# Performance work log

Hardware: AMD Instinct MI355X
Metric: run time of the kernel (lower is better)

## Reference

```python
import jax, jax.numpy as jnp
import numpy as np

N_NODES = 50000
N_EDGES = 100000
NUM_GRAPHS = 1024
EMB = 600
NUM_ATOMIC = 119      # Num_atomic_number
NUM_HYB = 8           # HybridizationType values
NUM_AROM = 2
NUM_CHIR = 4          # ChiralType values
NUM_CHARGE = 9
NUM_BOND_TYPE = 22    # BondType values


def setup_inputs() -> dict:
    key = jax.random.key(0)
    ks = jax.random.split(key, 20)
    # integer graph data
    atom = jnp.stack([
        jax.random.randint(ks[0], (N_NODES,), 0, NUM_ATOMIC),
        jax.random.randint(ks[1], (N_NODES,), 0, NUM_HYB),
        jax.random.randint(ks[2], (N_NODES,), 0, NUM_AROM),
        jax.random.randint(ks[3], (N_NODES,), 0, NUM_CHIR),
        jax.random.randint(ks[4], (N_NODES,), 0, NUM_CHARGE),
    ], axis=1)
    bond_index = jax.random.randint(ks[5], (2, N_EDGES), 0, N_NODES)
    bond_attr = jnp.stack([
        jax.random.randint(ks[6], (N_EDGES,), 0, NUM_BOND_TYPE),
        jax.random.randint(ks[7], (N_EDGES,), 0, NUM_ATOMIC),
    ], axis=1)
    batch = jnp.sort(jax.random.randint(ks[8], (N_NODES,), 0, NUM_GRAPHS))
    # parameters (kaiming-uniform-ish scale)
    def emb(k, n, d):
        bound = float(np.sqrt(6.0 / d))
        return jax.random.uniform(k, (n, d), minval=-bound, maxval=bound, dtype=jnp.float32)
    def lin(k, out_d, in_d):
        bound = float(np.sqrt(6.0 / in_d))
        return jax.random.uniform(k, (out_d, in_d), minval=-bound, maxval=bound, dtype=jnp.float32)
    return {
        "atom": atom, "bond_index": bond_index, "bond_attr": bond_attr, "batch": batch,
        "W_atom_num": emb(ks[9], NUM_ATOMIC, EMB),
        "W_hyb": emb(ks[10], NUM_HYB, EMB),
        "W_arom": emb(ks[11], NUM_AROM, EMB),
        "W_chir": emb(ks[12], NUM_CHIR, EMB),
        "W_charge": emb(ks[13], NUM_CHARGE, EMB),
        "W_bond_type": emb(ks[14], NUM_BOND_TYPE, EMB),
        "W_bond_atom_i": emb(ks[15], NUM_ATOMIC, EMB),
        "W_sl_atom": emb(ks[16], NUM_ATOMIC, EMB),
        "W_sl": emb(ks[17], 1, EMB),
        "W1": lin(ks[18], EMB, EMB), "b1": jnp.zeros((EMB,), jnp.float32),
        "W2": lin(ks[19], EMB // 2, EMB), "b2": jnp.zeros((EMB // 2,), jnp.float32),
        "W3": lin(jax.random.fold_in(key, 99), 1, EMB // 2),
    }


def reference(atom, bond_index, bond_attr, batch,
              W_atom_num, W_hyb, W_arom, W_chir, W_charge,
              W_bond_type, W_bond_atom_i, W_sl_atom, W_sl,
              W1, b1, W2, b2, W3):
    N = atom.shape[0]
    # Step 1: node embedding = sum of 5 lookups  [N, EMB]
    node = (W_atom_num[atom[:, 0]] + W_hyb[atom[:, 1]] + W_arom[atom[:, 2]]
            + W_chir[atom[:, 3]] + W_charge[atom[:, 4]])
    # Step 2: edge embeddings; self-loops appended after real bonds
    bond_emb = W_bond_type[bond_attr[:, 0]] + W_bond_atom_i[bond_attr[:, 1]]  # [E, EMB]
    sl_emb = W_sl_atom[atom[:, 0]] + W_sl[0]                                  # [N, EMB]
    edge_emb = jnp.concatenate([bond_emb, sl_emb], axis=0)                    # [E+N, EMB]
    loop = jnp.arange(N, dtype=bond_index.dtype)
    src = jnp.concatenate([bond_index[0], loop])
    dst = jnp.concatenate([bond_index[1], loop])
    # Step 3: 2 message-passing layers: gather src, multiply edge_emb, scatter-add to dst
    for _ in range(2):
        node = jax.ops.segment_sum(node[src] * edge_emb, dst, num_segments=N)
    # Step 4: energy MLP  ReLU -> Linear(d,d) -> ReLU -> Linear(d,d/2) -> ReLU -> Linear(d/2,1)
    h = jax.nn.relu(node)
    h = jax.nn.relu(h @ W1.T + b1)
    h = jax.nn.relu(h @ W2.T + b2)
    node_energy = h @ W3.T  # [N, 1]
    # Step 5: global add pool per graph
    dg = jax.ops.segment_sum(node_energy, batch, num_segments=NUM_GRAPHS)  # [NUM_GRAPHS, 1]
    return dg
```

## Files before the change

### kernel.cpp

```cpp
#include <hip/hip_runtime.h>

#define EMB 600
#define Q4  150
#define KP  608

typedef unsigned short ushortT;
typedef __attribute__((ext_vector_type(8))) short short8;
typedef __attribute__((ext_vector_type(4))) short short4v;
typedef __attribute__((ext_vector_type(4))) float f32x4;

__device__ __forceinline__ float4 f4add(float4 a, float4 b) {
    return make_float4(a.x + b.x, a.y + b.y, a.z + b.z, a.w + b.w);
}
__device__ __forceinline__ float4 f4fma(float4 acc, float4 v, float4 e) {
    return make_float4(fmaf(v.x, e.x, acc.x), fmaf(v.y, e.y, acc.y),
                       fmaf(v.z, e.z, acc.z), fmaf(v.w, e.w, acc.w));
}
__device__ __forceinline__ ushortT bf16_rne(float x) {
    unsigned u = __float_as_uint(x);
    return (ushortT)((u + 0x7fffu + ((u >> 16) & 1u)) >> 16);
}
__device__ __forceinline__ float bf16_to_f(ushortT h) {
    return __uint_as_float(((unsigned)h) << 16);
}
__device__ __forceinline__ short4v f4_to_bf4(float4 v) {
    short4v r;
    r[0] = (short)bf16_rne(v.x);
    r[1] = (short)bf16_rne(v.y);
    r[2] = (short)bf16_rne(v.z);
    r[3] = (short)bf16_rne(v.w);
    return r;
}
__device__ __forceinline__ float4 bf4_to_f4(short4v h) {
    return make_float4(bf16_to_f((ushortT)h[0]), bf16_to_f((ushortT)h[1]),
                       bf16_to_f((ushortT)h[2]), bf16_to_f((ushortT)h[3]));
}

__device__ __forceinline__ size_t frag_off(int row, int col) {
    return ((size_t)((row >> 4) * 19 + (col >> 5)) * 64
            + (row & 15) + 16 * ((col >> 3) & 3)) * 8 + (col & 7);
}

__global__ void k_node_embed_b(const int* __restrict__ atom,
                               const float4* __restrict__ Wa,
                               const float4* __restrict__ Wh,
                               const float4* __restrict__ War,
                               const float4* __restrict__ Wc,
                               const float4* __restrict__ Wch,
                               ushortT* __restrict__ out, int N) {
    int idx = blockIdx.x * blockDim.x + threadIdx.x;
    int total = N * Q4;
    if (idx >= total) return;
    int n = idx / Q4;
    int q = idx - n * Q4;
    const int* a = atom + n * 5;
    float4 r = Wa[a[0] * Q4 + q];
    r = f4add(r, Wh [a[1] * Q4 + q]);
    r = f4add(r, War[a[2] * Q4 + q]);
    r = f4add(r, Wc [a[3] * Q4 + q]);
    r = f4add(r, Wch[a[4] * Q4 + q]);
    *(short4v*)(out + (size_t)n * EMB + q * 4) = f4_to_bf4(r);
}

__global__ void k_hist(const int* __restrict__ bdst, int* __restrict__ counts, int E) {
    int i = blockIdx.x * blockDim.x + threadIdx.x;
    if (i < E) atomicAdd(&counts[bdst[i]], 1);
}

__global__ __launch_bounds__(256) void k_scan_l1(const int* __restrict__ counts,
                                                 int* __restrict__ offsets,
                                                 int* __restrict__ blocksums, int N) {
    __shared__ int s[256];
    int t = threadIdx.x;
    int i = blockIdx.x * 256 + t;
    int v = (i < N) ? counts[i] : 0;
    s[t] = v;
    __syncthreads();
#pragma unroll
    for (int off = 1; off < 256; off <<= 1) {
        int x = (t >= off) ? s[t - off] : 0;
        __syncthreads();
        s[t] += x;
        __syncthreads();
    }
    if (i < N) offsets[i] = s[t] - v;
    if (t == 255) blocksums[blockIdx.x] = s[255];
}

__global__ __launch_bounds__(256) void k_scan_l2(int* __restrict__ blocksums,
                                                 int* __restrict__ blockpref, int nb) {
    __shared__ int s[256];
    int t = threadIdx.x;
    int v = (t < nb) ? blocksums[t] : 0;
    s[t] = v;
    __syncthreads();
#pragma unroll
    for (int off = 1; off < 256; off <<= 1) {
        int x = (t >= off) ? s[t - off] : 0;
        __syncthreads();
        s[t] += x;
        __syncthreads();
    }
    if (t < nb) blockpref[t] = s[t] - v;
}

__global__ __launch_bounds__(256) void k_scan_l3(int* __restrict__ offsets,
                                                 int* __restrict__ cursor,
                                                 const int* __restrict__ blockpref, int N) {
    int i = blockIdx.x * 256 + threadIdx.x;
    if (i < N) {
        int o = offsets[i] + blockpref[blockIdx.x];
        offsets[i] = o;
        cursor[i]  = o;
    }
}

__global__ void k_scatter(const int* __restrict__ bdst, int* __restrict__ cursor,
                          int* __restrict__ edge_list, int E) {
    int i = blockIdx.x * blockDim.x + threadIdx.x;
    if (i < E) {
        int pos = atomicAdd(&cursor[bdst[i]], 1);
        edge_list[pos] = i;
    }
}

#define MP_BODY                                                                \
    int start = offsets[d], cnt = counts[d];                                   \
    int s0 = 0, t00 = 0, t01 = 0, s1 = 0, t10 = 0, t11 = 0;                    \
    if (cnt > 0) {                                                             \
        int e = edge_list[start];                                              \
        s0 = bsrc[e]; t00 = battr[2 * e]; t01 = battr[2 * e + 1];              \
    }                                                                          \
    if (cnt > 1) {                                                             \
        int e = edge_list[start + 1];                                          \
        s1 = bsrc[e]; t10 = battr[2 * e]; t11 = battr[2 * e + 1];              \
    }                                                                          \
    short4v cs1 = {0, 0, 0, 0}, cs2 = {0, 0, 0, 0};                            \
    if (cnt > 0) {                                                             \
        const ushortT* sr = in + (size_t)s0 * EMB;                             \
        cs1 = *(const short4v*)(sr + q1 * 4);                                  \
        if (has2) cs2 = *(const short4v*)(sr + q2 * 4);                        \
    }                                                                          \
    const float4* slA = Wsla + atom[d * 5] * Q4;                               \
    const ushortT* inr = in + (size_t)d * EMB;                                 \
    float4 acc1 = make_float4(0, 0, 0, 0), acc2 = acc1;                        \
    acc1 = f4fma(acc1, bf4_to_f4(*(const short4v*)(inr + q1 * 4)),             \
                 f4add(slA[q1], Wsl[q1]));                                     \
    if (has2) acc2 = f4fma(acc2, bf4_to_f4(*(const short4v*)(inr + q2 * 4)),   \
                           f4add(slA[q2], Wsl[q2]));                           \
    for (int k = 0; k < cnt; k++) {                                            \
        short4v xs1 = cs1, xs2 = cs2;                                          \
        int ct0 = t00, ct1 = t01;                                              \
        s0 = s1; t00 = t10; t01 = t11;                                         \
        if (k + 2 < cnt) {                                                     \
            int e = edge_list[start + k + 2];                                  \
            s1 = bsrc[e]; t10 = battr[2 * e]; t11 = battr[2 * e + 1];          \
        }                                                                      \
        if (k + 1 < cnt) {                                                     \
            const ushortT* sr = in + (size_t)s0 * EMB;                         \
            cs1 = *(const short4v*)(sr + q1 * 4);                              \
            if (has2) cs2 = *(const short4v*)(sr + q2 * 4);                    \
        }                                                                      \
        const float4* e0 = Wbt  + ct0 * Q4;                                    \
        const float4* e1 = Wbai + ct1 * Q4;                                    \
        acc1 = f4fma(acc1, bf4_to_f4(xs1), f4add(e0[q1], e1[q1]));             \
        if (has2) acc2 = f4fma(acc2, bf4_to_f4(xs2), f4add(e0[q2], e1[q2]));   \
    }

__global__ __launch_bounds__(256) void k_mp_gather_b(
        const int* __restrict__ bsrc, const int* __restrict__ battr,
        const int* __restrict__ atom,
        const int* __restrict__ offsets, const int* __restrict__ counts,
        const int* __restrict__ edge_list,
        const float4* __restrict__ Wbt, const float4* __restrict__ Wbai,
        const float4* __restrict__ Wsla, const float4* __restrict__ Wsl,
        const ushortT* __restrict__ in, ushortT* __restrict__ out, int N) {
    int wid  = (int)((blockIdx.x * blockDim.x + threadIdx.x) >> 6);
    int lane = threadIdx.x & 63;
    int d    = wid >> 1;
    int half = wid & 1;
    if (d >= N) return;
    int q1 = 75 * half + lane;
    int q2 = q1 + 64;
    bool has2 = lane < 11;

    MP_BODY

    ushortT* orow = out + (size_t)d * EMB;
    *(short4v*)(orow + q1 * 4) = f4_to_bf4(acc1);
    if (has2) *(short4v*)(orow + q2 * 4) = f4_to_bf4(acc2);
}

__device__ __forceinline__ void frag_store4h(ushortT* __restrict__ hi,
                                             int d, int q, float4 v) {
    int kc = q >> 3, ks = (q >> 1) & 3, halfw = q & 1;
    size_t off = ((size_t)((d >> 4) * 19 + kc) * 64 + (d & 15) + 16 * ks) * 8
                 + halfw * 4;
    float vv[4] = {v.x, v.y, v.z, v.w};
    short4v h4;
#pragma unroll
    for (int j = 0; j < 4; j++)
        h4[j] = (short)bf16_rne(fmaxf(vv[j], 0.f));
    *(short4v*)(hi + off) = h4;
}

__global__ __launch_bounds__(256) void k_mp_gather_rs(
        const int* __restrict__ bsrc, const int* __restrict__ battr,
        const int* __restrict__ atom,
        const int* __restrict__ offsets, const int* __restrict__ counts,
        const int* __restrict__ edge_list,
        const float4* __restrict__ Wbt, const float4* __restrict__ Wbai,
        const float4* __restrict__ Wsla, const float4* __restrict__ Wsl,
        const ushortT* __restrict__ in,
        ushortT* __restrict__ hi, int N) {
    int wid  = (int)((blockIdx.x * blockDim.x + threadIdx.x) >> 6);
    int lane = threadIdx.x & 63;
    int d    = wid >> 1;
    int half = wid & 1;
    if (d >= N) return;
    int q1 = 75 * half + lane;
    int q2 = q1 + 64;
    bool has2 = lane < 11;

    MP_BODY

    frag_store4h(hi, d, q1, acc1);
    if (has2) frag_store4h(hi, d, q2, acc2);
    if (half == 0 && lane == 31) {
        size_t off = ((size_t)((d >> 4) * 19 + 18) * 64 + (d & 15) + 48) * 8;
        short8 z = {0, 0, 0, 0, 0, 0, 0, 0};
        *(short8*)(hi + off) = z;
    }
}

__global__ void k_split_w_frag(const float* __restrict__ src,
                               short8* __restrict__ dst,
                               int rows_in, int cb_count) {
    int idx = blockIdx.x * blockDim.x + threadIdx.x;
    int total = cb_count * 19 * 64;
    if (idx >= total) return;
    int lane = idx & 63;
    int tile = idx >> 6;
    int cb = tile / 19, kc = tile - cb * 19;
    int col = cb * 16 + (lane & 15);
    int k0  = kc * 32 + (lane >> 4) * 8;
    short8 h;
#pragma unroll
    for (int j = 0; j < 8; j++) {
        int k = k0 + j;
        float x = (col < rows_in && k < 600) ? src[(size_t)col * 600 + k] : 0.f;
        h[j] = (short)bf16_rne(x);
    }
    dst[idx] = h;
}

struct FragSet { short8 a[4], b[4]; };

__device__ __forceinline__ void frag_load(FragSet& f,
        const short8* __restrict__ Af, const short8* __restrict__ Bf,
        int aBase, int bBase, int kc) {
    int ak = aBase + kc * 64;
    int bk = bBase + kc * 64;
#pragma unroll
    for (int i = 0; i < 4; i++) {
        f.a[i] = Af[ak + i * 1216];
        f.b[i] = Bf[bk + i * 1216];
    }
}

__device__ __forceinline__ void frag_mfma(const FragSet& f, f32x4 acc[4][4]) {
#pragma unroll
    for (int i = 0; i < 4; i++)
#pragma unroll
        for (int j = 0; j < 4; j++)
            acc[i][j] = __builtin_amdgcn_mfma_f32_16x16x32_bf16(f.a[i], f.b[j], acc[i][j], 0, 0, 0);
}

__device__ __forceinline__ void gemm_core_reg(
        const short8* __restrict__ Af, const short8* __restrict__ Bf,
        int aBase, int bBase, f32x4 acc[4][4]) {
    for (int kc = 0; kc < 19; kc++) {
        FragSet f;
        frag_load(f, Af, Bf, aBase, bBase, kc);
        frag_mfma(f, acc);
    }
}

__device__ __forceinline__ void decode_wg(int ncb, int& rowblk, int& colblk) {
    int nwg  = gridDim.x;
    int orig = blockIdx.x;
    int q = nwg >> 3, r = nwg & 7;
    int xcd = orig & 7, rank = orig >> 3;
    int wgid = (xcd < r ? xcd * (q + 1) : r * (q + 1) + (xcd - r) * q) + rank;
    rowblk = wgid / ncb;
    colblk = wgid - rowblk * ncb;
}

__global__ __launch_bounds__(256, 4) void k_gemm1r(
        const short8* __restrict__ Af, const short8* __restrict__ Wf,
        const float* __restrict__ b1,
        ushortT* __restrict__ Hf, int N) {
    int rowblk, colblk;
    decode_wg(5, rowblk, colblk);
    int row0 = rowblk * 128;
    int col0 = colblk * 128;
    int t = threadIdx.x, w = t >> 6, l = t & 63;
    int wr = w >> 1, wc = w & 1, fr = l & 15, fq = l >> 4;

    int aBase = (rowblk * 8 + wr * 4) * 1216 + l;
    int bBase = (colblk * 8 + wc * 4) * 1216 + l;
    f32x4 acc[4][4];
#pragma unroll
    for (int i = 0; i < 4; i++)
#pragma unroll
        for (int j = 0; j < 4; j++) acc[i][j] = f32x4{0.f, 0.f, 0.f, 0.f};
    gemm_core_reg(Af, Wf, aBase, bBase, acc);

#pragma unroll
    for (int i = 0; i < 4; i++) {
#pragma unroll
        for (int j = 0; j < 4; j++) {
            int col = col0 + wc * 64 + j * 16 + fr;
            float bias = (col < 600) ? b1[col] : 0.f;
#pragma unroll
            for (int r = 0; r < 4; r++) {
                int row = row0 + wr * 64 + i * 16 + fq * 4 + r;
                if (row >= N) continue;
                if (col < 600) {
                    float x = fmaxf(acc[i][j][r] + bias, 0.f);
                    Hf[frag_off(row, col)] = bf16_rne(x);
                } else if (col < KP) {
                    Hf[frag_off(row, col)] = 0;
                }
            }
        }
    }
}

__global__ __launch_bounds__(256, 4) void k_gemm2r(
        const short8* __restrict__ Af, const short8* __restrict__ Wf,
        const float* __restrict__ b2, const float* __restrict__ W3,
        float* __restrict__ energy, int N) {
    __shared__ float sE[128];
    int rowblk, colblk;
    decode_wg(3, rowblk, colblk);
    int row0 = rowblk * 128;
    int col0 = colblk * 128;
    int t = threadIdx.x, w = t >> 6, l = t & 63;
    int wr = w >> 1, wc = w & 1, fr = l & 15, fq = l >> 4;

    int aBase = (rowblk * 8 + wr * 4) * 1216 + l;
    int bBase = (colblk * 8 + wc * 4) * 1216 + l;
    f32x4 acc[4][4];
#pragma unroll
    for (int i = 0; i < 4; i++)
#pragma unroll
        for (int j = 0; j < 4; j++) acc[i][j] = f32x4{0.f, 0.f, 0.f, 0.f};
    gemm_core_reg(Af, Wf, aBase, bBase, acc);

    if (t < 128) sE[t] = 0.f;
    __syncthreads();
#pragma unroll
    for (int i = 0; i < 4; i++) {
        float p[4] = {0.f, 0.f, 0.f, 0.f};
#pragma unroll
        for (int j = 0; j < 4; j++) {
            int col = col0 + wc * 64 + j * 16 + fr;
            if (col < 300) {
                float bias = b2[col];
                float wv   = W3[col];
#pragma unroll
                for (int r = 0; r < 4; r++)
                    p[r] += fmaxf(acc[i][j][r] + bias, 0.f) * wv;
            }
        }
#pragma unroll
        for (int r = 0; r < 4; r++) {
            float v = p[r];
            v += __shfl_xor(v, 1, 64);
            v += __shfl_xor(v, 2, 64);
            v += __shfl_xor(v, 4, 64);
            v += __shfl_xor(v, 8, 64);
            p[r] = v;
        }
        if (fr == 0) {
#pragma unroll
            for (int r = 0; r < 4; r++)
                atomicAdd(&sE[wr * 64 + i * 16 + fq * 4 + r], p[r]);
        }
    }
    __syncthreads();
    if (t < 128) {
        int row = row0 + t;
        if (row < N) atomicAdd(&energy[row], sE[t]);
    }
}

__global__ void k_pool(const float* __restrict__ energy, const int* __restrict__ batch,
                       float* __restrict__ dg, int N) {
    int i = blockIdx.x * blockDim.x + threadIdx.x;
    int lane = threadIdx.x & 63;
    float v = (i < N) ? energy[i] : 0.f;
    int   b = (i < N) ? batch[i]  : -1;
#pragma unroll
    for (int off = 1; off < 64; off <<= 1) {
        float vv = __shfl_down(v, off, 64);
        int   bb = __shfl_down(b, off, 64);
        if (lane + off < 64 && bb == b) v += vv;
    }
    int pb = __shfl_up(b, 1, 64);
    if (i < N && (lane == 0 || pb != b)) atomicAdd(&dg[b], v);
}

extern "C" void kernel_launch(void* const* d_in, const int* in_sizes, int n_in,
                              void* d_out, int out_size, void* d_ws, size_t ws_size,
                              hipStream_t stream) {
    const int* atom       = (const int*)d_in[0];
    const int* bond_index = (const int*)d_in[1];
    const int* bond_attr  = (const int*)d_in[2];
    const int* batch      = (const int*)d_in[3];
    const float* Wa   = (const float*)d_in[4];
    const float* Wh   = (const float*)d_in[5];
    const float* War  = (const float*)d_in[6];
    const float* Wc   = (const float*)d_in[7];
    const float* Wch  = (const float*)d_in[8];
    const float* Wbt  = (const float*)d_in[9];
    const float* Wbai = (const float*)d_in[10];
    const float* Wsla = (const float*)d_in[11];
    const float* Wsl  = (const float*)d_in[12];
    const float* W1   = (const float*)d_in[13];
    const float* b1   = (const float*)d_in[14];
    const float* W2   = (const float*)d_in[15];
    const float* b2   = (const float*)d_in[16];
    const float* W3   = (const float*)d_in[17];

    int N = in_sizes[0] / 5;
    int E = in_sizes[1] / 2;
    int Mb = (N + 127) / 128;
    int Npad = Mb * 128;
    int nTiles = Npad / 16;
    int nb = (N + 255) / 256;

    size_t regionBytes = (size_t)Npad * KP * 4;
    char* base = (char*)d_ws;
    ushortT* nodeAb = (ushortT*)base;
    ushortT* nodeBh = (ushortT*)(base + regionBytes);
    short8* Af = (short8*)nodeAb;
    short8* Hf = (short8*)nodeBh;
    char* tail = base + 2 * regionBytes;
    float* energy  = (float*)tail;
    int* counts    = (int*)(energy + N);
    int* offsets   = counts + N;
    int* cursor    = offsets + N;
    int* edge_list = cursor + N;
    short8* W1f    = (short8*)(edge_list + E);
    short8* W2f    = W1f + 40 * 19 * 64;
    int* blocksums = (int*)(W2f + 24 * 19 * 64);
    int* blockpref = blocksums + 256;

    const int* bsrc = bond_index;
    const int* bdst = bond_index + E;

    hipMemsetAsync(counts, 0, (size_t)N * sizeof(int), stream);
    k_hist<<<(E + 255) / 256, 256, 0, stream>>>(bdst, counts, E);
    k_scan_l1<<<nb, 256, 0, stream>>>(counts, offsets, blocksums, N);
    k_scan_l2<<<1, 256, 0, stream>>>(blocksums, blockpref, nb);
    k_scan_l3<<<nb, 256, 0, stream>>>(offsets, cursor, blockpref, N);
    k_scatter<<<(E + 255) / 256, 256, 0, stream>>>(bdst, cursor, edge_list, E);

    k_split_w_frag<<<(40 * 19 * 64 + 255) / 256, 256, 0, stream>>>(W1, W1f, 600, 40);
    k_split_w_frag<<<(24 * 19 * 64 + 255) / 256, 256, 0, stream>>>(W2, W2f, 300, 24);

    {
        int total = N * Q4;
        k_node_embed_b<<<(total + 255) / 256, 256, 0, stream>>>(
            atom, (const float4*)Wa, (const float4*)Wh, (const float4*)War,
            (const float4*)Wc, (const float4*)Wch, nodeAb, N);
    }

    int mpblocks = (2 * N * 64 + 255) / 256;
    k_mp_gather_b<<<mpblocks, 256, 0, stream>>>(bsrc, bond_attr, atom,
        offsets, counts, edge_list,
        (const float4*)Wbt, (const float4*)Wbai, (const float4*)Wsla, (const float4*)Wsl,
        nodeAb, nodeBh, N);

    {
        int firstPad = N / 16;
        size_t offB  = (size_t)firstPad * 1216 * 16;
        size_t cntB  = (size_t)(nTiles - firstPad) * 1216 * 16;
        if (cntB) hipMemsetAsync((char*)Af + offB, 0, cntB, stream);
    }

    k_mp_gather_rs<<<mpblocks, 256, 0, stream>>>(bsrc, bond_attr, atom,
        offsets, counts, edge_list,
        (const float4*)Wbt, (const float4*)Wbai, (const float4*)Wsla, (const float4*)Wsl,
        nodeBh, (ushortT*)Af, N);

    k_gemm1r<<<Mb * 5, 256, 0, stream>>>(Af, W1f, b1, (ushortT*)Hf, N);

    hipMemsetAsync(energy, 0, (size_t)N * sizeof(float), stream);
    k_gemm2r<<<Mb * 3, 256, 0, stream>>>(Hf, W2f, b2, W3, energy, N);

    hipMemsetAsync(d_out, 0, (size_t)out_size * sizeof(float), stream);
    k_pool<<<(N + 255) / 256, 256, 0, stream>>>(energy, batch, (float*)d_out, N);
}
```

Before: 344.6 us.

## Precompute bf16 combined bond-embedding table and flatten edge lists in CSR

Builds a bf16 table holding every (bond_type, bond_atom) sum of embeddings, plus a bf16 self-loop table, so each edge in message passing reads one combined row instead of two fp32 rows plus an add. The scatter now writes source index and combo index straight into CSR order, which removes the edge_list indirection and the battr gathers. This adds two small precompute kernels and a table of about 22*119 rows. It also rounds the edge embeddings to bf16, which adds precision error.

```diff
diff --git a/kernel.cpp b/kernel.cpp
--- a/kernel.cpp
+++ b/kernel.cpp
@@ -39,6 +39,35 @@
 __device__ __forceinline__ size_t frag_off(int row, int col) {
     return ((size_t)((row >> 4) * 19 + (col >> 5)) * 64
             + (row & 15) + 16 * ((col >> 3) & 3)) * 8 + (col & 7);
+}
+
+__global__ void k_combo(const float* __restrict__ Wbt, const float* __restrict__ Wbai,
+                        ushortT* __restrict__ dst, int rBAI, int total) {
+    int idx = blockIdx.x * blockDim.x + threadIdx.x;
+    if (idx >= total) return;
+    int row = idx / 75, u = idx - row * 75;
+    int bt = row / rBAI, bai = row - bt * rBAI;
+    const float* pa = Wbt  + (size_t)bt  * EMB + u * 8;
+    const float* pb = Wbai + (size_t)bai * EMB + u * 8;
+    short8 h;
+#pragma unroll
+    for (int j = 0; j < 8; j++)
+        h[j] = (short)bf16_rne(pa[j] + pb[j]);
+    *(short8*)(dst + (size_t)row * EMB + u * 8) = h;
+}
+
+__global__ void k_slc(const float* __restrict__ Wsla, const float* __restrict__ Wsl,
+                      ushortT* __restrict__ dst, int total) {
+    int idx = blockIdx.x * blockDim.x + threadIdx.x;
+    if (idx >= total) return;
+    int row = idx / 75, u = idx - row * 75;
+    const float* pa = Wsla + (size_t)row * EMB + u * 8;
+    const float* pb = Wsl + u * 8;
+    short8 h;
+#pragma unroll
+    for (int j = 0; j < 8; j++)
+        h[j] = (short)bf16_rne(pa[j] + pb[j]);
+    *(short8*)(dst + (size_t)row * EMB + u * 8) = h;
 }
 
 __global__ void k_node_embed_b(const int* __restrict__ atom,
@@ -115,65 +144,59 @@
     }
 }
 
-__global__ void k_scatter(const int* __restrict__ bdst, int* __restrict__ cursor,
-                          int* __restrict__ edge_list, int E) {
+__global__ void k_scatter2(const int* __restrict__ bsrc, const int* __restrict__ bdst,
+                           const int* __restrict__ battr, int* __restrict__ cursor,
+                           int* __restrict__ src_list, int* __restrict__ cidx_list,
+                           int E, int rBAI) {
     int i = blockIdx.x * blockDim.x + threadIdx.x;
     if (i < E) {
         int pos = atomicAdd(&cursor[bdst[i]], 1);
-        edge_list[pos] = i;
+        src_list[pos]  = bsrc[i];
+        cidx_list[pos] = battr[2 * i] * rBAI + battr[2 * i + 1];
     }
 }
 
 #define MP_BODY                                                                \
     int start = offsets[d], cnt = counts[d];                                   \
-    int s0 = 0, t00 = 0, t01 = 0, s1 = 0, t10 = 0, t11 = 0;                    \
-    if (cnt > 0) {                                                             \
-        int e = edge_list[start];                                              \
-        s0 = bsrc[e]; t00 = battr[2 * e]; t01 = battr[2 * e + 1];              \
-    }                                                                          \
-    if (cnt > 1) {                                                             \
-        int e = edge_list[start + 1];                                          \
-        s1 = bsrc[e]; t10 = battr[2 * e]; t11 = battr[2 * e + 1];              \
-    }                                                                          \
+    int s0 = 0, c0 = 0, s1 = 0, c1 = 0;                                        \
+    if (cnt > 0) { s0 = src_list[start]; c0 = cidx_list[start]; }              \
+    if (cnt > 1) { s1 = src_list[start + 1]; c1 = cidx_list[start + 1]; }      \
     short4v cs1 = {0, 0, 0, 0}, cs2 = {0, 0, 0, 0};                            \
     if (cnt > 0) {                                                             \
         const ushortT* sr = in + (size_t)s0 * EMB;                             \
         cs1 = *(const short4v*)(sr + q1 * 4);                                  \
         if (has2) cs2 = *(const short4v*)(sr + q2 * 4);                        \
     }                                                                          \
-    const float4* slA = Wsla + atom[d * 5] * Q4;                               \
+    const ushortT* slA = Tslc + (size_t)atom[d * 5] * EMB;                     \
     const ushortT* inr = in + (size_t)d * EMB;                                 \
     float4 acc1 = make_float4(0, 0, 0, 0), acc2 = acc1;                        \
     acc1 = f4fma(acc1, bf4_to_f4(*(const short4v*)(inr + q1 * 4)),             \
-                 f4add(slA[q1], Wsl[q1]));                                     \
+                 bf4_to_f4(*(const short4v*)(slA + q1 * 4)));                  \
     if (has2) acc2 = f4fma(acc2, bf4_to_f4(*(const short4v*)(inr + q2 * 4)),   \
-                           f4add(slA[q2], Wsl[q2]));                           \
+                           bf4_to_f4(*(const short4v*)(slA + q2 * 4)));        \
     for (int k = 0; k < cnt; k++) {                                            \
         short4v xs1 = cs1, xs2 = cs2;                                          \
-        int ct0 = t00, ct1 = t01;                                              \
-        s0 = s1; t00 = t10; t01 = t11;                                         \
-        if (k + 2 < cnt) {                                                     \
-            int e = edge_list[start + k + 2];                                  \
-            s1 = bsrc[e]; t10 = battr[2 * e]; t11 = battr[2 * e + 1];          \
-        }                                                                      \
+        int cc = c0;                                                           \
+        s0 = s1; c0 = c1;                                                      \
+        if (k + 2 < cnt) { s1 = src_list[start + k + 2];                       \
+                           c1 = cidx_list[start + k + 2]; }                    \
         if (k + 1 < cnt) {                                                     \
             const ushortT* sr = in + (size_t)s0 * EMB;                         \
             cs1 = *(const short4v*)(sr + q1 * 4);                              \
             if (has2) cs2 = *(const short4v*)(sr + q2 * 4);                    \
         }                                                                      \
-        const float4* e0 = Wbt  + ct0 * Q4;                                    \
-        const float4* e1 = Wbai + ct1 * Q4;                                    \
-        acc1 = f4fma(acc1, bf4_to_f4(xs1), f4add(e0[q1], e1[q1]));             \
-        if (has2) acc2 = f4fma(acc2, bf4_to_f4(xs2), f4add(e0[q2], e1[q2]));   \
+        const ushortT* ce = Tcombo + (size_t)cc * EMB;                         \
+        acc1 = f4fma(acc1, bf4_to_f4(xs1),                                     \
+                     bf4_to_f4(*(const short4v*)(ce + q1 * 4)));               \
+        if (has2) acc2 = f4fma(acc2, bf4_to_f4(xs2),                           \
+                     bf4_to_f4(*(const short4v*)(ce + q2 * 4)));               \
     }
 
 __global__ __launch_bounds__(256) void k_mp_gather_b(
-        const int* __restrict__ bsrc, const int* __restrict__ battr,
+        const int* __restrict__ src_list, const int* __restrict__ cidx_list,
         const int* __restrict__ atom,
         const int* __restrict__ offsets, const int* __restrict__ counts,
-        const int* __restrict__ edge_list,
-        const float4* __restrict__ Wbt, const float4* __restrict__ Wbai,
-        const float4* __restrict__ Wsla, const float4* __restrict__ Wsl,
+        const ushortT* __restrict__ Tcombo, const ushortT* __restrict__ Tslc,
         const ushortT* __restrict__ in, ushortT* __restrict__ out, int N) {
     int wid  = (int)((blockIdx.x * blockDim.x + threadIdx.x) >> 6);
     int lane = threadIdx.x & 63;
@@ -205,12 +228,10 @@
 }
 
 __global__ __launch_bounds__(256) void k_mp_gather_rs(
-        const int* __restrict__ bsrc, const int* __restrict__ battr,
+        const int* __restrict__ src_list, const int* __restrict__ cidx_list,
         const int* __restrict__ atom,
         const int* __restrict__ offsets, const int* __restrict__ counts,
-        const int* __restrict__ edge_list,
-        const float4* __restrict__ Wbt, const float4* __restrict__ Wbai,
-        const float4* __restrict__ Wsla, const float4* __restrict__ Wsl,
+        const ushortT* __restrict__ Tcombo, const ushortT* __restrict__ Tslc,
         const ushortT* __restrict__ in,
         ushortT* __restrict__ hi, int N) {
     int wid  = (int)((blockIdx.x * blockDim.x + threadIdx.x) >> 6);
@@ -436,6 +457,10 @@
 
     int N = in_sizes[0] / 5;
     int E = in_sizes[1] / 2;
+    int rBT  = in_sizes[9]  / EMB;
+    int rBAI = in_sizes[10] / EMB;
+    int rSLA = in_sizes[11] / EMB;
+    int NCOMBO = rBT * rBAI;
     int Mb = (N + 127) / 128;
     int Npad = Mb * 128;
     int nTiles = Npad / 16;
@@ -452,11 +477,14 @@
     int* counts    = (int*)(energy + N);
     int* offsets   = counts + N;
     int* cursor    = offsets + N;
-    int* edge_list = cursor + N;
-    short8* W1f    = (short8*)(edge_list + E);
+    int* src_list  = cursor + N;
+    int* cidx_list = src_list + E;
+    short8* W1f    = (short8*)(cidx_list + E);
     short8* W2f    = W1f + 40 * 19 * 64;
     int* blocksums = (int*)(W2f + 24 * 19 * 64);
     int* blockpref = blocksums + 256;
+    ushortT* Tcombo = (ushortT*)(blockpref + 256);
+    ushortT* Tslc   = Tcombo + (size_t)NCOMBO * EMB;
 
     const int* bsrc = bond_index;
     const int* bdst = bond_index + E;
@@ -466,7 +494,15 @@
     k_scan_l1<<<nb, 256, 0, stream>>>(counts, offsets, blocksums, N);
     k_scan_l2<<<1, 256, 0, stream>>>(blocksums, blockpref, nb);
     k_scan_l3<<<nb, 256, 0, stream>>>(offsets, cursor, blockpref, N);
-    k_scatter<<<(E + 255) / 256, 256, 0, stream>>>(bdst, cursor, edge_list, E);
+    k_scatter2<<<(E + 255) / 256, 256, 0, stream>>>(bsrc, bdst, bond_attr, cursor,
+                                                    src_list, cidx_list, E, rBAI);
+
+    {
+        int tot = NCOMBO * 75;
+        k_combo<<<(tot + 255) / 256, 256, 0, stream>>>(Wbt, Wbai, Tcombo, rBAI, tot);
+        tot = rSLA * 75;
+        k_slc<<<(tot + 255) / 256, 256, 0, stream>>>(Wsla, Wsl, Tslc, tot);
+    }
 
     k_split_w_frag<<<(40 * 19 * 64 + 255) / 256, 256, 0, stream>>>(W1, W1f, 600, 40);
     k_split_w_frag<<<(24 * 19 * 64 + 255) / 256, 256, 0, stream>>>(W2, W2f, 300, 24);
@@ -479,10 +515,8 @@
     }
 
     int mpblocks = (2 * N * 64 + 255) / 256;
-    k_mp_gather_b<<<mpblocks, 256, 0, stream>>>(bsrc, bond_attr, atom,
-        offsets, counts, edge_list,
-        (const float4*)Wbt, (const float4*)Wbai, (const float4*)Wsla, (const float4*)Wsl,
-        nodeAb, nodeBh, N);
+    k_mp_gather_b<<<mpblocks, 256, 0, stream>>>(src_list, cidx_list, atom,
+        offsets, counts, Tcombo, Tslc, nodeAb, nodeBh, N);
 
     {
         int firstPad = N / 16;
@@ -491,10 +525,8 @@
         if (cntB) hipMemsetAsync((char*)Af + offB, 0, cntB, stream);
     }
 
-    k_mp_gather_rs<<<mpblocks, 256, 0, stream>>>(bsrc, bond_attr, atom,
-        offsets, counts, edge_list,
-        (const float4*)Wbt, (const float4*)Wbai, (const float4*)Wsla, (const float4*)Wsl,
-        nodeBh, (ushortT*)Af, N);
+    k_mp_gather_rs<<<mpblocks, 256, 0, stream>>>(src_list, cidx_list, atom,
+        offsets, counts, Tcombo, Tslc, nodeBh, (ushortT*)Af, N);
 
     k_gemm1r<<<Mb * 5, 256, 0, stream>>>(Af, W1f, b1, (ushortT*)Hf, N);
 
```

After: 314.9 us, median of 2. 8.6% less time.
